# Kernel optimization log

Hardware: AMD Instinct MI355X
Metric: run time of the kernel (lower is better)

Reference implementation:

```python
import jax, jax.numpy as jnp
import numpy as np

N = 30000        # nodes
E = 600000       # edges
R = 32           # relations
NB = 30          # num_bases
D = 128          # entity_dim == hidden_dim == output_dim
H = 8            # heads, head dim C = D // H = 16
NUM_ENT = 100000
NGRAPH = 16      # graphs in batch
L = 2            # num_rgcn_layers == num_transformer_layers
EPS = 1e-5


def _ln(x, g, b):
    mu = x.mean(-1, keepdims=True)
    var = ((x - mu) ** 2).mean(-1, keepdims=True)
    return (x - mu) * jax.lax.rsqrt(var + EPS) * g + b


def setup_inputs() -> dict:
    key = jax.random.key(0)
    ks = iter(jax.random.split(key, 48))

    def nrm(shape, s=0.05):
        return jax.random.normal(next(ks), shape, jnp.float32) * s

    inp = {}
    inp["node_ids"] = jax.random.randint(next(ks), (N,), 0, NUM_ENT)
    inp["edge_index"] = jax.random.randint(next(ks), (2, E), 0, N)
    inp["edge_type"] = jax.random.randint(next(ks), (E,), 0, R)
    inp["batch"] = jnp.sort(jax.random.randint(next(ks), (N,), 0, NGRAPH))
    inp["entity_emb"] = nrm((NUM_ENT, D)).at[0].set(0.0)  # padding_idx=0
    inp["rel_emb"] = nrm((R, D)).at[0].set(0.0)           # padding_idx=0
    inp["rgcn_comp"] = nrm((L, R, NB))
    inp["rgcn_bases"] = nrm((L, NB, D, D))
    inp["rgcn_root"] = nrm((L, D, D))
    inp["rgcn_bias"] = jnp.zeros((L, D), jnp.float32)
    inp["rgcn_ln_g"] = jnp.ones((L, D), jnp.float32)
    inp["rgcn_ln_b"] = jnp.zeros((L, D), jnp.float32)
    inp["tr_wq"] = nrm((L, D, D)); inp["tr_bq"] = jnp.zeros((L, D), jnp.float32)
    inp["tr_wk"] = nrm((L, D, D)); inp["tr_bk"] = jnp.zeros((L, D), jnp.float32)
    inp["tr_wv"] = nrm((L, D, D)); inp["tr_bv"] = jnp.zeros((L, D), jnp.float32)
    inp["tr_we"] = nrm((L, D, D))                          # lin_edge (bias=False in PyG)
    inp["tr_wskip"] = nrm((L, D, D)); inp["tr_bskip"] = jnp.zeros((L, D), jnp.float32)
    inp["tr_ln_g"] = jnp.ones((L, D), jnp.float32)
    inp["tr_ln_b"] = jnp.zeros((L, D), jnp.float32)
    return inp


def reference(node_ids, edge_index, edge_type, batch, entity_emb, rel_emb,
              rgcn_comp, rgcn_bases, rgcn_root, rgcn_bias, rgcn_ln_g, rgcn_ln_b,
              tr_wq, tr_bq, tr_wk, tr_bk, tr_wv, tr_bv, tr_we, tr_wskip, tr_bskip,
              tr_ln_g, tr_ln_b):
    src, tgt = edge_index[0], edge_index[1]
    C = D // H
    x = entity_emb[node_ids]            # [N, D]
    edge_attr = rel_emb[edge_type]      # [E, D]

    # ---- RGCN layers: basis decomposition, mean aggregation per (target, relation) ----
    seg = tgt * R + edge_type
    cnt = jax.ops.segment_sum(jnp.ones((E,), jnp.float32), seg, num_segments=N * R)
    inv = jnp.where(cnt > 0, 1.0 / jnp.maximum(cnt, 1.0), 0.0)   # [N*R]
    for l in range(L):
        agg = jax.ops.segment_sum(x[src], seg, num_segments=N * R)   # [N*R, D]
        agg = (agg * inv[:, None]).reshape(N, R, D)
        w = jnp.einsum('rb,bio->rio', rgcn_comp[l], rgcn_bases[l])   # [R, D, D]
        x = jnp.einsum('nri,rio->no', agg, w) + x @ rgcn_root[l] + rgcn_bias[l]
        x = jax.nn.relu(_ln(x, rgcn_ln_g[l], rgcn_ln_b[l]))          # dropout = identity (eval)

    # ---- TransformerConv layers: edge-conditioned multi-head attention ----
    for l in range(L):
        q = (x @ tr_wq[l] + tr_bq[l]).reshape(N, H, C)
        k = (x @ tr_wk[l] + tr_bk[l]).reshape(N, H, C)
        v = (x @ tr_wv[l] + tr_bv[l]).reshape(N, H, C)
        e = (edge_attr @ tr_we[l]).reshape(E, H, C)
        kj = k[src] + e                                              # [E, H, C]
        vj = v[src] + e
        alpha = jnp.einsum('ehc,ehc->eh', q[tgt], kj) / np.float32(np.sqrt(C))
        m = jax.ops.segment_max(alpha, tgt, num_segments=N)          # [N, H]
        a = jnp.exp(alpha - m[tgt])
        denom = jax.ops.segment_sum(a, tgt, num_segments=N)
        a = a / jnp.maximum(denom[tgt], 1e-16)                       # softmax per target node
        out = jax.ops.segment_sum((vj * a[:, :, None]).reshape(E, D), tgt, num_segments=N)
        out = out + x @ tr_wskip[l] + tr_bskip[l]                    # root/skip connection
        out = jax.nn.relu(_ln(out, tr_ln_g[l], tr_ln_b[l]))          # dropout = identity (eval)
        x = x + out                                                  # dims match -> residual

    cnt_g = jax.ops.segment_sum(jnp.ones((N,), jnp.float32), batch, num_segments=NGRAPH)
    graph_emb = jax.ops.segment_sum(x, batch, num_segments=NGRAPH) / jnp.maximum(cnt_g, 1.0)[:, None]
    return x, graph_emb
```

## Files before the change

### kernel.cpp

```cpp
#include <hip/hip_runtime.h>

#define NN 30000
#define NE 600000
#define RR 32
#define NBASE 30
#define NG 16

typedef long long i64;
typedef unsigned short ushort;
typedef short bf16x8 __attribute__((ext_vector_type(8)));
typedef float f32x4 __attribute__((ext_vector_type(4)));

__device__ __forceinline__ ushort f2bf(float f){
  unsigned u = __float_as_uint(f);
  u += 0x7fffu + ((u >> 16) & 1u);
  return (ushort)(u >> 16);
}
__device__ __forceinline__ float bf2f(ushort u){
  return __uint_as_float(((unsigned)u) << 16);
}
__device__ __forceinline__ unsigned pk2(float a, float b){
  return (unsigned)f2bf(a) | ((unsigned)f2bf(b) << 16);
}

__global__ void k_gather(const float* __restrict__ emb, const int* __restrict__ ids,
                         float* __restrict__ x, ushort* __restrict__ xb){
  int t = blockIdx.x*256 + threadIdx.x;
  if (t >= NN*32) return;
  int n = t >> 5, c = t & 31;
  float4 v = ((const float4*)emb)[(i64)ids[n]*32 + c];
  ((float4*)x)[(i64)n*32 + c] = v;
  *(uint2*)&xb[(i64)n*128 + c*4] = make_uint2(pk2(v.x, v.y), pk2(v.z, v.w));
}

__global__ void k_cnt(const int* __restrict__ tgt, const int* __restrict__ ety,
                      float* __restrict__ cnt){
  int e = blockIdx.x*256 + threadIdx.x;
  if (e >= NE) return;
  atomicAdd(&cnt[(i64)tgt[e]*RR + ety[e]], 1.0f);
}

__global__ void k_hist_blk(const int* __restrict__ ety, int* __restrict__ hist){
  __shared__ int lh[RR];
  if (threadIdx.x < RR) lh[threadIdx.x] = 0;
  __syncthreads();
  int e0 = blockIdx.x*2048 + threadIdx.x;
  #pragma unroll
  for (int i = 0; i < 8; i++){
    int e = e0 + i*256;
    if (e < NE) atomicAdd(&lh[ety[e]], 1);
  }
  __syncthreads();
  if (threadIdx.x < RR){
    int v = lh[threadIdx.x];
    if (v) atomicAdd(&hist[threadIdx.x], v);
  }
}

__global__ void k_scan(const int* __restrict__ hist, int* __restrict__ base,
                       int* __restrict__ cursor, int* __restrict__ pb,
                       int* __restrict__ pb64){
  if (threadIdx.x != 0 || blockIdx.x != 0) return;
  int s = 0, p = 0, p64 = 0;
  for (int r = 0; r < RR; r++){
    base[r] = s; cursor[r] = s; pb[r] = p; pb64[r] = p64;
    s += hist[r]; p += (hist[r] + 127) >> 7; p64 += (hist[r] + 63) >> 6;
  }
  base[RR] = s; pb[RR] = p; pb64[RR] = p64;
}

__global__ __launch_bounds__(256) void k_scatter_blk(const int* __restrict__ ety,
    int* __restrict__ cursor, int* __restrict__ eord){
  __shared__ int lh[RR];
  __shared__ int lb[RR];
  if (threadIdx.x < RR) lh[threadIdx.x] = 0;
  __syncthreads();
  int e0 = blockIdx.x*2048 + threadIdx.x;
  #pragma unroll
  for (int i = 0; i < 8; i++){
    int e = e0 + i*256;
    if (e < NE) atomicAdd(&lh[ety[e]], 1);
  }
  __syncthreads();
  if (threadIdx.x < RR){
    int c = lh[threadIdx.x];
    lb[threadIdx.x] = c ? atomicAdd(&cursor[threadIdx.x], c) : 0;
  }
  __syncthreads();
  if (threadIdx.x < RR) lh[threadIdx.x] = 0;
  __syncthreads();
  #pragma unroll
  for (int i = 0; i < 8; i++){
    int e = e0 + i*256;
    if (e < NE){
      int r = ety[e];
      int loc = atomicAdd(&lh[r], 1);
      eord[lb[r] + loc] = e;
    }
  }
}

__global__ void k_hist2(const int* __restrict__ etgt, int* __restrict__ hist2){
  int e = blockIdx.x*256 + threadIdx.x;
  if (e >= NE) return;
  atomicAdd(&hist2[etgt[e]], 1);
}

__global__ __launch_bounds__(1024) void k_scan2(const int* __restrict__ hist2,
    int* __restrict__ rowptr, int* __restrict__ cursor2){
  __shared__ int s[1024];
  int t = threadIdx.x;
  int base = t*30;
  int loc[30];
  int sum = 0;
  #pragma unroll
  for (int i = 0; i < 30; i++){
    int v = (base+i < NN) ? hist2[base+i] : 0;
    loc[i] = sum; sum += v;
  }
  s[t] = sum; __syncthreads();
  for (int off = 1; off < 1024; off <<= 1){
    int v = (t >= off) ? s[t-off] : 0;
    __syncthreads();
    s[t] += v;
    __syncthreads();
  }
  int excl = (t > 0) ? s[t-1] : 0;
  #pragma unroll
  for (int i = 0; i < 30; i++){
    int idx = base + i;
    if (idx <= NN){
      rowptr[idx] = excl + loc[i];
      if (idx < NN) cursor2[idx] = excl + loc[i];
    }
  }
}

__global__ void k_scatter2(const int* __restrict__ etgt, const int* __restrict__ esrc,
                           const int* __restrict__ ety, int* __restrict__ cursor2,
                           int2* __restrict__ se2, int* __restrict__ pos2){
  int e = blockIdx.x*256 + threadIdx.x;
  if (e >= NE) return;
  int q = atomicAdd(&cursor2[etgt[e]], 1);
  se2[q] = make_int2(esrc[e], ety[e]);
  pos2[e] = q;
  if (e == 0){
    se2[NE]     = make_int2(0, 0);
    se2[NE + 1] = make_int2(0, 0);
  }
}

__global__ void k_prep(const int* __restrict__ eord, const int* __restrict__ esrc,
                       const int* __restrict__ etgt, const int* __restrict__ ety,
                       const int* __restrict__ pos2, const float* __restrict__ cnt,
                       int* __restrict__ sg_src, int* __restrict__ sg_p2,
                       float* __restrict__ sg_inv){
  int s = blockIdx.x*256 + threadIdx.x;
  if (s >= NE) return;
  int eid = eord[s];
  sg_src[s] = esrc[eid];
  sg_p2[s]  = pos2[eid];
  sg_inv[s] = 1.0f / cnt[(i64)etgt[eid]*RR + ety[eid]];
}

__global__ void k_basis(const float* __restrict__ comp, const float* __restrict__ bases,
                        float* __restrict__ wT, ushort* __restrict__ wTb){
  int t = blockIdx.x*256 + threadIdx.x;
  int r = t >> 14, rem = t & 16383, c = rem >> 7, kk = rem & 127;
  float acc = 0.f;
  for (int b = 0; b < NBASE; b++)
    acc += comp[r*NBASE + b] * bases[(i64)b*16384 + kk*128 + c];
  wT[t] = acc;
  wTb[t] = f2bf(acc);
}

__global__ void k_tw(const float* __restrict__ root, const float* __restrict__ wq,
                     const float* __restrict__ wk, const float* __restrict__ wv,
                     const float* __restrict__ wsk, ushort* __restrict__ out){
  int z = blockIdx.y;
  const float* srcs[5] = {root, wq, wk, wv, wsk};
  const float* S = srcs[z >> 1] + (i64)(z & 1)*16384;
  int idx = blockIdx.x*256 + threadIdx.x;
  int c = idx >> 7, kk = idx & 127;
  out[(i64)z*16384 + idx] = f2bf(S[kk*128 + c]);
}


__global__ __launch_bounds__(256, 4) void k_mm_mfma(const ushort* __restrict__ xb,
    const ushort* __restrict__ wTb, const float* __restrict__ bias,
    float* __restrict__ Y, int nrows){
  __shared__ ushort Xs[16384];
  int t = threadIdx.x;
  int row0 = blockIdx.x * 128;
  for (int i = t; i < 2048; i += 256){
    int row = i >> 4, c = i & 15;
    int gr = min(row0 + row, nrows - 1);
    *(uint4*)((char*)Xs + row*256 + ((c*16) ^ ((row&7)<<4))) =
        *(const uint4*)((const char*)(xb + (i64)gr*128) + c*16);
  }
  __syncthreads();
  int w = t >> 6, l = t & 63;
  int wm = w >> 1, wn = w & 1;
  int lrow = l & 15, lg = l >> 4;
  int swz = (lrow & 7) << 4;
  const char* pX = (const char*)Xs + (wm*64 + lrow)*256;
  const char* pW = (const char*)wTb + (wn*64 + lrow)*256 + 16*lg;
  f32x4 acc[4][4] = {};
  #pragma unroll
  for (int ks = 0; ks < 4; ks++){
    int kb = (16*lg + 64*ks) ^ swz;
    bf16x8 a[4], bx[4];
    #pragma unroll
    for (int ns = 0; ns < 4; ns++) a[ns]  = *(const bf16x8*)(pW + ns*4096 + 64*ks);
    #pragma unroll
    for (int ms = 0; ms < 4; ms++) bx[ms] = *(const bf16x8*)(pX + ms*4096 + kb);
    #pragma unroll
    for (int ms = 0; ms < 4; ms++)
      #pragma unroll
      for (int ns = 0; ns < 4; ns++)
        acc[ms][ns] = __builtin_amdgcn_mfma_f32_16x16x32_bf16(a[ns], bx[ms], acc[ms][ns], 0, 0, 0);
  }
  #pragma unroll
  for (int ms = 0; ms < 4; ms++){
    int m = row0 + wm*64 + ms*16 + lrow;
    if (m >= nrows) continue;
    #pragma unroll
    for (int ns = 0; ns < 4; ns++){
      int n0 = wn*64 + ns*16 + 4*lg;
      float4 bv = *(const float4*)&bias[n0];
      f32x4 v = acc[ms][ns];
      *(float4*)&Y[(i64)m*128 + n0] =
          make_float4(v[0]+bv.x, v[1]+bv.y, v[2]+bv.z, v[3]+bv.w);
    }
  }
}

__global__ __launch_bounds__(256, 4) void k_mm4(const ushort* __restrict__ xb,
    const ushort* __restrict__ wTb, int layer,
    const float* __restrict__ biq, const float* __restrict__ bik,
    const float* __restrict__ biv, const float* __restrict__ bisk,
    ushort* __restrict__ qo, ushort* __restrict__ ko, ushort* __restrict__ vo,
    float* __restrict__ z, int nrows){
  __shared__ ushort Xs[16384];
  int t = threadIdx.x;
  int row0 = blockIdx.x * 128;
  for (int i = t; i < 2048; i += 256){
    int row = i >> 4, c = i & 15;
    int gr = min(row0 + row, nrows - 1);
    *(uint4*)((char*)Xs + row*256 + ((c*16) ^ ((row&7)<<4))) =
        *(const uint4*)((const char*)(xb + (i64)gr*128) + c*16);
  }
  __syncthreads();
  int w = t >> 6, l = t & 63;
  int wm = w >> 1, wn = w & 1;
  int lrow = l & 15, lg = l >> 4;
  int swz = (lrow & 7) << 4;
  const char* pX = (const char*)Xs + (wm*64 + lrow)*256;
  const float* biases[4] = {biq, bik, biv, bisk};
  ushort* outs[3] = {qo, ko, vo};
  #pragma unroll 1
  for (int arr = 0; arr < 4; arr++){
    const char* pW = (const char*)(wTb + (i64)(2 + 2*arr + layer)*16384)
                     + (wn*64 + lrow)*256 + 16*lg;
    f32x4 acc[4][4] = {};
    #pragma unroll
    for (int ks = 0; ks < 4; ks++){
      int kb = (16*lg + 64*ks) ^ swz;
      bf16x8 a[4], bx[4];
      #pragma unroll
      for (int ns = 0; ns < 4; ns++) a[ns]  = *(const bf16x8*)(pW + ns*4096 + 64*ks);
      #pragma unroll
      for (int ms = 0; ms < 4; ms++) bx[ms] = *(const bf16x8*)(pX + ms*4096 + kb);
      #pragma unroll
      for (int ms = 0; ms < 4; ms++)
        #pragma unroll
        for (int ns = 0; ns < 4; ns++)
          acc[ms][ns] = __builtin_amdgcn_mfma_f32_16x16x32_bf16(a[ns], bx[ms], acc[ms][ns], 0, 0, 0);
    }
    const float* bias = biases[arr];
    #pragma unroll
    for (int ms = 0; ms < 4; ms++){
      int m = row0 + wm*64 + ms*16 + lrow;
      if (m >= nrows) continue;
      #pragma unroll
      for (int ns = 0; ns < 4; ns++){
        int n0 = wn*64 + ns*16 + 4*lg;
        float4 bv = *(const float4*)&bias[n0];
        f32x4 v = acc[ms][ns];
        if (arr < 3){
          *(uint2*)&outs[arr][(i64)m*128 + n0] =
              make_uint2(pk2(v[0]+bv.x, v[1]+bv.y), pk2(v[2]+bv.z, v[3]+bv.w));
        } else {
          *(float4*)&z[(i64)m*128 + n0] =
              make_float4(v[0]+bv.x, v[1]+bv.y, v[2]+bv.z, v[3]+bv.w);
        }
      }
    }
  }
}

__global__ __launch_bounds__(256, 4) void k_edge_mfma(
    const int* __restrict__ sg_src, const int* __restrict__ sg_p2,
    const float* __restrict__ sg_inv, const int* __restrict__ hist,
    const int* __restrict__ base, const int* __restrict__ pb,
    const ushort* __restrict__ xb, const ushort* __restrict__ wb,
    ushort* __restrict__ y){
  __shared__ ushort Xs[16384];
  __shared__ int s_src[128];
  __shared__ int s_p2[128];
  __shared__ float s_inv[128];
  int b = blockIdx.x;
  int r = -1;
  #pragma unroll 1
  for (int i = 0; i < RR; i++){
    if (b >= pb[i] && b < pb[i+1]) { r = i; break; }
  }
  if (r < 0) return;
  int chunk = b - pb[r];
  int rowbase = base[r] + chunk*128;
  int nvalid = min(128, hist[r] - chunk*128);
  int t = threadIdx.x;
  if (t < 128){
    bool valid = t < nvalid;
    int slot = rowbase + (valid ? t : 0);
    s_src[t] = sg_src[slot];
    s_p2[t]  = valid ? sg_p2[slot] : NE;
    s_inv[t] = valid ? sg_inv[slot] : 0.0f;
  }
  __syncthreads();
  for (int i = t; i < 2048; i += 256){
    int row = i >> 4, c = i & 15;
    *(uint4*)((char*)Xs + row*256 + ((c*16) ^ ((row&7)<<4))) =
        *(const uint4*)((const char*)(xb + (i64)s_src[row]*128) + c*16);
  }
  __syncthreads();
  int w = t >> 6, l = t & 63;
  int wm = w >> 1, wn = w & 1;
  int lrow = l & 15, lg = l >> 4;
  int swz = (lrow & 7) << 4;
  const char* pX = (const char*)Xs + (wm*64 + lrow)*256;
  const char* pW = (const char*)(wb + (i64)r*16384) + (wn*64 + lrow)*256 + 16*lg;
  f32x4 acc[4][4] = {};
  #pragma unroll
  for (int ks = 0; ks < 4; ks++){
    int kb = (16*lg + 64*ks) ^ swz;
    bf16x8 a[4], bx[4];
    #pragma unroll
    for (int ns = 0; ns < 4; ns++) a[ns]  = *(const bf16x8*)(pW + ns*4096 + 64*ks);
    #pragma unroll
    for (int ms = 0; ms < 4; ms++) bx[ms] = *(const bf16x8*)(pX + ms*4096 + kb);
    #pragma unroll
    for (int ms = 0; ms < 4; ms++)
      #pragma unroll
      for (int ns = 0; ns < 4; ns++)
        acc[ms][ns] = __builtin_amdgcn_mfma_f32_16x16x32_bf16(a[ns], bx[ms], acc[ms][ns], 0, 0, 0);
  }
  __syncthreads();
  #pragma unroll
  for (int ms = 0; ms < 4; ms++){
    int m = wm*64 + ms*16 + lrow;
    float sc = s_inv[m];
    int msk = (m & 7) << 4;
    #pragma unroll
    for (int ns = 0; ns < 4; ns++){
      int n0 = wn*64 + ns*16 + 4*lg;
      f32x4 v = acc[ms][ns];
      *(uint2*)((char*)Xs + m*256 + ((n0*2) ^ msk)) =
          make_uint2(pk2(v[0]*sc, v[1]*sc), pk2(v[2]*sc, v[3]*sc));
    }
  }
  __syncthreads();
  for (int i = t; i < 2048; i += 256){
    int row = i >> 4, c = i & 15;
    uint4 v = *(const uint4*)((const char*)Xs + row*256 + ((c*16) ^ ((row&7)<<4)));
    *(uint4*)&y[(i64)s_p2[row]*128 + c*8] = v;
  }
}

__global__ __launch_bounds__(256) void k_edge_atomic(const int* __restrict__ esrc,
    const int* __restrict__ etgt, const int* __restrict__ eord,
    const int* __restrict__ hist, const int* __restrict__ base,
    const int* __restrict__ pb, const float* __restrict__ cnt,
    const float* __restrict__ x, const float* __restrict__ wT,
    float* __restrict__ z){
  __shared__ float Xs[64][132];
  __shared__ int s_src[64];
  __shared__ int s_tgt[64];
  __shared__ float s_inv[64];
  int b = blockIdx.x;
  int r = -1;
  #pragma unroll 1
  for (int i = 0; i < RR; i++){
    if (b >= pb[i] && b < pb[i+1]) { r = i; break; }
  }
  if (r < 0) return;
  int chunk = b - pb[r];
  int rowbase = base[r] + chunk*64;
  int cnt_r = hist[r];
  if (threadIdx.x < 64){
    int i = threadIdx.x;
    bool valid = (chunk*64 + i) < cnt_r;
    int eid = valid ? eord[rowbase + i] : 0;
    int sv = valid ? esrc[eid] : 0;
    int tv = valid ? etgt[eid] : 0;
    s_src[i] = sv; s_tgt[i] = tv;
    s_inv[i] = valid ? (1.0f / cnt[(i64)tv*RR + r]) : 0.0f;
  }
  __syncthreads();
  for (int idx = threadIdx.x; idx < 64*32; idx += 256){
    int rr = idx >> 5, c4 = idx & 31;
    *(float4*)&Xs[rr][c4*4] = ((const float4*)x)[(i64)s_src[rr]*32 + c4];
  }
  __syncthreads();
  const float* W = wT + (i64)r*16384;
  int m = threadIdx.x & 15, cg = threadIdx.x >> 4;
  float acc[4][8] = {};
  #pragma unroll 2
  for (int k4 = 0; k4 < 128; k4 += 4){
    float4 xv[4], wv[8];
    #pragma unroll
    for (int i = 0; i < 4; i++) xv[i] = *(float4*)&Xs[m + 16*i][k4];
    #pragma unroll
    for (int j = 0; j < 8; j++) wv[j] = *(const float4*)&W[(i64)(cg + 16*j)*128 + k4];
    #pragma unroll
    for (int i = 0; i < 4; i++)
      #pragma unroll
      for (int j = 0; j < 8; j++)
        acc[i][j] += xv[i].x*wv[j].x + xv[i].y*wv[j].y + xv[i].z*wv[j].z + xv[i].w*wv[j].w;
  }
  #pragma unroll
  for (int i = 0; i < 4; i++){
    int rr = m + 16*i;
    float sc = s_inv[rr];
    i64 o = (i64)s_tgt[rr]*128;
    #pragma unroll
    for (int j = 0; j < 8; j++)
      atomicAdd(&z[o + cg + 16*j], acc[i][j]*sc);
  }
}

__global__ void k_seg(const int* __restrict__ rowptr, const ushort* __restrict__ y,
                      const float* __restrict__ z, const float* __restrict__ g,
                      const float* __restrict__ b, float* __restrict__ x,
                      ushort* __restrict__ xb){
  int t = (blockIdx.x*256 + threadIdx.x) >> 6;
  int l = threadIdx.x & 63;
  if (t >= NN) return;
  int q0 = rowptr[t], q1 = rowptr[t+1];
  float ax = 0.f, ay = 0.f;
  for (int q = q0; q < q1; q++){
    ushort2 u = *(const ushort2*)&y[(i64)q*128 + 2*l];
    ax += bf2f(u.x); ay += bf2f(u.y);
  }
  float2 zv = *(const float2*)&z[(i64)t*128 + 2*l];
  float tx = ax + zv.x, ty = ay + zv.y;
  float s = tx + ty;
  #pragma unroll
  for (int o = 1; o < 64; o <<= 1) s += __shfl_xor(s, o);
  float mu = s * 0.0078125f;
  float dx = tx - mu, dy = ty - mu;
  float s2 = dx*dx + dy*dy;
  #pragma unroll
  for (int o = 1; o < 64; o <<= 1) s2 += __shfl_xor(s2, o);
  float rs = rsqrtf(s2 * 0.0078125f + 1e-5f);
  float2 gg = *(const float2*)&g[2*l];
  float2 bb = *(const float2*)&b[2*l];
  float o0 = fmaxf(dx*rs*gg.x + bb.x, 0.f);
  float o1 = fmaxf(dy*rs*gg.y + bb.y, 0.f);
  *(float2*)&x[(i64)t*128 + 2*l] = make_float2(o0, o1);
  *(unsigned*)&xb[(i64)t*128 + 2*l] = pk2(o0, o1);
}

__global__ void k_lnrelu(const float* __restrict__ z, const float* __restrict__ g,
                         const float* __restrict__ b, float* __restrict__ xo,
                         ushort* __restrict__ xb){
  int w = (blockIdx.x*256 + threadIdx.x) >> 6;
  int l = threadIdx.x & 63;
  if (w >= NN) return;
  float2 v = *(const float2*)&z[(i64)w*128 + 2*l];
  float s = v.x + v.y;
  #pragma unroll
  for (int o = 1; o < 64; o <<= 1) s += __shfl_xor(s, o);
  float mu = s * 0.0078125f;
  float dx = v.x - mu, dy = v.y - mu;
  float s2 = dx*dx + dy*dy;
  #pragma unroll
  for (int o = 1; o < 64; o <<= 1) s2 += __shfl_xor(s2, o);
  float rs = rsqrtf(s2 * 0.0078125f + 1e-5f);
  float2 gg = *(const float2*)&g[2*l];
  float2 bb = *(const float2*)&b[2*l];
  float o0 = fmaxf(dx*rs*gg.x + bb.x, 0.f);
  float o1 = fmaxf(dy*rs*gg.y + bb.y, 0.f);
  *(float2*)&xo[(i64)w*128 + 2*l] = make_float2(o0, o1);
  *(unsigned*)&xb[(i64)w*128 + 2*l] = pk2(o0, o1);
}

__global__ void k_ew(const float* __restrict__ rel, const float* __restrict__ we,
                     float* __restrict__ ew){
  int t = blockIdx.x*256 + threadIdx.x;
  int r = t >> 7, c = t & 127;
  float acc = 0.f;
  for (int k = 0; k < 128; k++) acc += rel[r*128 + k] * we[k*128 + c];
  ew[t] = acc;
}

__global__ __launch_bounds__(256) void k_attn(const int2* __restrict__ se2,
    const int* __restrict__ rowptr,
    const ushort* __restrict__ qbb, const ushort* __restrict__ kbb,
    const ushort* __restrict__ vbb, const float* __restrict__ ew,
    const float* __restrict__ sk, const float* __restrict__ g,
    const float* __restrict__ b, float* __restrict__ x, ushort* __restrict__ xb){
  __shared__ float sew[RR*128];
  __shared__ float part[4][3][64];
  for (int i = threadIdx.x; i < RR*32; i += 256)
    ((float4*)sew)[i] = ((const float4*)ew)[i];
  __syncthreads();
  int wid = threadIdx.x >> 6;
  int half = wid & 1;
  int t = blockIdx.x*2 + (wid >> 1);
  int l = threadIdx.x & 63;
  int q0 = rowptr[t], q1 = rowptr[t+1];
  unsigned qu = *(const unsigned*)&qbb[(i64)t*128 + 2*l];
  float qx = bf2f((ushort)qu) * 0.25f, qy = bf2f((ushort)(qu >> 16)) * 0.25f;
  float den = 0.f, ox = 0.f, oy = 0.f;
  int qs = q0 + half;
  if (qs < q1){
    int2 sr = se2[qs];
    unsigned ku = *(const unsigned*)&kbb[(i64)sr.x*128 + 2*l];
    unsigned vu = *(const unsigned*)&vbb[(i64)sr.x*128 + 2*l];
    int r = sr.y;
    for (int q = qs; q < q1; q += 2){
      int2 srn = se2[q + 2];
      unsigned kun = *(const unsigned*)&kbb[(i64)srn.x*128 + 2*l];
      unsigned vun = *(const unsigned*)&vbb[(i64)srn.x*128 + 2*l];
      float2 ev = *(const float2*)&sew[r*128 + 2*l];
      float kx = bf2f((ushort)ku) + ev.x, ky = bf2f((ushort)(ku >> 16)) + ev.y;
      float p = qx*kx + qy*ky;
      p += __shfl_xor(p, 1); p += __shfl_xor(p, 2); p += __shfl_xor(p, 4);
      float wgt = __expf(p);
      den += wgt;
      ox += wgt*(bf2f((ushort)vu) + ev.x);
      oy += wgt*(bf2f((ushort)(vu >> 16)) + ev.y);
      ku = kun; vu = vun; r = srn.y;
    }
  }
  part[wid][0][l] = ox; part[wid][1][l] = oy; part[wid][2][l] = den;
  __syncthreads();
  if (half) return;
  ox  += part[wid^1][0][l];
  oy  += part[wid^1][1][l];
  den += part[wid^1][2][l];
  float dn = fmaxf(den, 1e-16f);
  float2 zv = *(const float2*)&sk[(i64)t*128 + 2*l];
  float tx = ox/dn + zv.x, ty = oy/dn + zv.y;
  float s = tx + ty;
  #pragma unroll
  for (int o = 1; o < 64; o <<= 1) s += __shfl_xor(s, o);
  float mu = s * 0.0078125f;
  float dx = tx - mu, dy = ty - mu;
  float s2 = dx*dx + dy*dy;
  #pragma unroll
  for (int o = 1; o < 64; o <<= 1) s2 += __shfl_xor(s2, o);
  float rs = rsqrtf(s2 * 0.0078125f + 1e-5f);
  float2 gg = *(const float2*)&g[2*l];
  float2 bb = *(const float2*)&b[2*l];
  float o0 = fmaxf(dx*rs*gg.x + bb.x, 0.f);
  float o1 = fmaxf(dy*rs*gg.y + bb.y, 0.f);
  float2 xv = *(const float2*)&x[(i64)t*128 + 2*l];
  float nx = xv.x + o0, ny = xv.y + o1;
  *(float2*)&x[(i64)t*128 + 2*l] = make_float2(nx, ny);
  *(unsigned*)&xb[(i64)t*128 + 2*l] = pk2(nx, ny);
}

__global__ void k_copy(const float* __restrict__ x, float* __restrict__ out){
  int t = blockIdx.x*256 + threadIdx.x;
  if (t >= NN*32) return;
  ((float4*)out)[t] = ((const float4*)x)[t];
}

__global__ void k_cntg(const int* __restrict__ batch, float* __restrict__ cntg){
  __shared__ int lh[NG];
  if (threadIdx.x < NG) lh[threadIdx.x] = 0;
  __syncthreads();
  int n = blockIdx.x*256 + threadIdx.x;
  if (n < NN) atomicAdd(&lh[batch[n]], 1);
  __syncthreads();
  if (threadIdx.x < NG){
    int v = lh[threadIdx.x];
    if (v) atomicAdd(&cntg[threadIdx.x], (float)v);
  }
}

__global__ void k_pool(const float* __restrict__ x, const int* __restrict__ batch,
                       float* __restrict__ gsum){
  __shared__ float acc[NG*128];
  for (int i = threadIdx.x; i < NG*128; i += 256) acc[i] = 0.f;
  __syncthreads();
  int per = (NN + gridDim.x - 1) / gridDim.x;
  int n0 = blockIdx.x*per, n1 = min(n0 + per, NN);
  int sub = threadIdx.x >> 5, c4 = threadIdx.x & 31;
  for (int n = n0 + sub; n < n1; n += 8){
    int g = batch[n];
    float4 xv = ((const float4*)x)[(i64)n*32 + c4];
    atomicAdd(&acc[g*128 + c4*4 + 0], xv.x);
    atomicAdd(&acc[g*128 + c4*4 + 1], xv.y);
    atomicAdd(&acc[g*128 + c4*4 + 2], xv.z);
    atomicAdd(&acc[g*128 + c4*4 + 3], xv.w);
  }
  __syncthreads();
  for (int i = threadIdx.x; i < NG*128; i += 256) atomicAdd(&gsum[i], acc[i]);
}

__global__ void k_poolfin(const float* __restrict__ gsum, const float* __restrict__ cntg,
                          float* __restrict__ gout){
  int t = blockIdx.x*256 + threadIdx.x;
  int g = t >> 7;
  gout[t] = gsum[t] / fmaxf(cntg[g], 1.0f);
}

extern "C" void kernel_launch(void* const* d_in, const int* in_sizes, int n_in,
                              void* d_out, int out_size, void* d_ws, size_t ws_size,
                              hipStream_t stream) {
  const int*   node_ids = (const int*)d_in[0];
  const int*   eidx  = (const int*)d_in[1];
  const int*   esrc  = eidx;
  const int*   etgt  = eidx + NE;
  const int*   ety   = (const int*)d_in[2];
  const int*   batch = (const int*)d_in[3];
  const float* ent   = (const float*)d_in[4];
  const float* rel   = (const float*)d_in[5];
  const float* comp  = (const float*)d_in[6];
  const float* bases = (const float*)d_in[7];
  const float* root  = (const float*)d_in[8];
  const float* rbias = (const float*)d_in[9];
  const float* rlng  = (const float*)d_in[10];
  const float* rlnb  = (const float*)d_in[11];
  const float* wq    = (const float*)d_in[12];
  const float* bq    = (const float*)d_in[13];
  const float* wk    = (const float*)d_in[14];
  const float* bk    = (const float*)d_in[15];
  const float* wv    = (const float*)d_in[16];
  const float* bv    = (const float*)d_in[17];
  const float* we    = (const float*)d_in[18];
  const float* wsk   = (const float*)d_in[19];
  const float* bsk   = (const float*)d_in[20];
  const float* tlng  = (const float*)d_in[21];
  const float* tlnb  = (const float*)d_in[22];
  float* out = (float*)d_out;

  char* wp = (char*)d_ws;
  auto alloc = [&](size_t bytes)->void*{
    void* p = (void*)wp;
    wp += (bytes + 255) & ~(size_t)255;
    return p;
  };
  float*    x     = (float*)alloc((size_t)NN*128*4);
  ushort*   xb    = (ushort*)alloc((size_t)NN*128*2);
  float*    z     = (float*)alloc((size_t)NN*128*4);
  ushort*   qbb   = (ushort*)alloc((size_t)NN*128*2);
  ushort*   kbb   = (ushort*)alloc((size_t)NN*128*2);
  ushort*   vbb   = (ushort*)alloc((size_t)NN*128*2);
  float*    cnt   = (float*)alloc((size_t)NN*RR*4);
  float*    wbT   = (float*)alloc((size_t)RR*16384*4);
  ushort*   wbTb  = (ushort*)alloc((size_t)RR*16384*2);
  ushort*   wTb   = (ushort*)alloc((size_t)10*16384*2);
  float*    ew    = (float*)alloc((size_t)RR*128*4);
  int*      eord  = (int*)alloc((size_t)NE*4);
  int*      pos2  = (int*)alloc((size_t)NE*4);
  int2*     se2   = (int2*)alloc((size_t)(NE + 2)*8);
  int*      sg_src= (int*)alloc((size_t)NE*4);
  int*      sg_p2 = (int*)alloc((size_t)NE*4);
  float*    sg_inv= (float*)alloc((size_t)NE*4);
  int*      hist  = (int*)alloc(RR*4);
  int*      base  = (int*)alloc((RR+1)*4);
  int*      cursor= (int*)alloc(RR*4);
  int*      pb    = (int*)alloc((RR+1)*4);
  int*      pb64  = (int*)alloc((RR+1)*4);
  int*      hist2 = (int*)alloc((size_t)NN*4);
  int*      rowptr= (int*)alloc((size_t)(NN+1)*4);
  int*      cursor2=(int*)alloc((size_t)NN*4);
  float*    cntg  = (float*)alloc(NG*4);
  float*    gsum  = (float*)alloc((size_t)NG*128*4);
  size_t ybytes = (size_t)(NE + 8)*128*2;
  ushort*   y     = (ushort*)alloc(ybytes);
  bool fast = ((char*)y + ybytes) <= ((char*)d_ws + ws_size);

  dim3 B(256);

  hipMemsetAsync(cnt, 0, (size_t)NN*RR*4, stream);
  hipMemsetAsync(hist, 0, RR*4, stream);
  hipMemsetAsync(hist2, 0, (size_t)NN*4, stream);

  k_gather<<<3750, B, 0, stream>>>(ent, node_ids, x, xb);
  k_cnt<<<2344, B, 0, stream>>>(etgt, ety, cnt);
  k_hist_blk<<<294, B, 0, stream>>>(ety, hist);
  k_scan<<<1, 1, 0, stream>>>(hist, base, cursor, pb, pb64);
  k_scatter_blk<<<294, B, 0, stream>>>(ety, cursor, eord);
  k_hist2<<<2344, B, 0, stream>>>(etgt, hist2);
  k_scan2<<<1, 1024, 0, stream>>>(hist2, rowptr, cursor2);
  k_scatter2<<<2344, B, 0, stream>>>(etgt, esrc, ety, cursor2, se2, pos2);
  k_prep<<<2344, B, 0, stream>>>(eord, esrc, etgt, ety, pos2, cnt, sg_src, sg_p2, sg_inv);
  k_tw<<<dim3(64,10), B, 0, stream>>>(root, wq, wk, wv, wsk, wTb);

  for (int l = 0; l < 2; l++){
    k_basis<<<2048, B, 0, stream>>>(comp + l*RR*NBASE, bases + (i64)l*NBASE*16384, wbT, wbTb);
    k_mm_mfma<<<235, B, 0, stream>>>(xb, wTb + (i64)(0 + l)*16384, rbias + l*128, z, NN);
    if (fast){
      k_edge_mfma<<<4720, B, 0, stream>>>(sg_src, sg_p2, sg_inv, hist, base, pb, xb, wbTb, y);
      k_seg<<<7500, B, 0, stream>>>(rowptr, y, z, rlng + l*128, rlnb + l*128, x, xb);
    } else {
      k_edge_atomic<<<9407, B, 0, stream>>>(esrc, etgt, eord, hist, base, pb64, cnt, x, wbT, z);
      k_lnrelu<<<7500, B, 0, stream>>>(z, rlng + l*128, rlnb + l*128, x, xb);
    }
  }

  for (int l = 0; l < 2; l++){
    k_ew<<<16, B, 0, stream>>>(rel, we + (i64)l*16384, ew);
    k_mm4<<<235, B, 0, stream>>>(xb, wTb, l, bq + l*128, bk + l*128, bv + l*128,
                                 bsk + l*128, qbb, kbb, vbb, z, NN);
    k_attn<<<15000, B, 0, stream>>>(se2, rowptr, qbb, kbb, vbb, ew, z,
                                    tlng + l*128, tlnb + l*128, x, xb);
  }

  k_copy<<<3750, B, 0, stream>>>(x, out);
  hipMemsetAsync(gsum, 0, (size_t)NG*128*4, stream);
  hipMemsetAsync(cntg, 0, NG*4, stream);
  k_cntg<<<118, B, 0, stream>>>(batch, cntg);
  k_pool<<<120, B, 0, stream>>>(x, batch, gsum);
  k_poolfin<<<8, B, 0, stream>>>(gsum, cntg, out + (i64)NN*128);
}
```

Baseline: 899.1 us.

## Fuse preprocessing kernels, deepen attention prefetch, write final layer to output

Merges the count, relation histogram and target histogram kernels into one pass, folds the small relation scan into the node scan, and folds the sorted-edge gather into the relation scatter kernel, cutting several launches and extra passes over the edge arrays. The attention kernel now prefetches four edges ahead instead of one to hide gather latency, with the padding of se2 grown to match. The last attention layer writes straight to the output buffer, which removes the final copy kernel. The deeper prefetch raises register use in the attention kernel.

After: 865.5 us. 3.7% less time.

```diff
diff --git a/kernel.cpp b/kernel.cpp
--- a/kernel.cpp
+++ b/kernel.cpp
@@ -33,14 +33,9 @@
   *(uint2*)&xb[(i64)n*128 + c*4] = make_uint2(pk2(v.x, v.y), pk2(v.z, v.w));
 }
 
-__global__ void k_cnt(const int* __restrict__ tgt, const int* __restrict__ ety,
-                      float* __restrict__ cnt){
-  int e = blockIdx.x*256 + threadIdx.x;
-  if (e >= NE) return;
-  atomicAdd(&cnt[(i64)tgt[e]*RR + ety[e]], 1.0f);
-}
-
-__global__ void k_hist_blk(const int* __restrict__ ety, int* __restrict__ hist){
+__global__ __launch_bounds__(256) void k_stats(const int* __restrict__ etgt,
+    const int* __restrict__ ety, float* __restrict__ cnt,
+    int* __restrict__ hist, int* __restrict__ hist2){
   __shared__ int lh[RR];
   if (threadIdx.x < RR) lh[threadIdx.x] = 0;
   __syncthreads();
@@ -48,7 +43,12 @@
   #pragma unroll
   for (int i = 0; i < 8; i++){
     int e = e0 + i*256;
-    if (e < NE) atomicAdd(&lh[ety[e]], 1);
+    if (e < NE){
+      int tgt = etgt[e], r = ety[e];
+      atomicAdd(&lh[r], 1);
+      atomicAdd(&hist2[tgt], 1);
+      atomicAdd(&cnt[(i64)tgt*RR + r], 1.0f);
+    }
   }
   __syncthreads();
   if (threadIdx.x < RR){
@@ -57,65 +57,26 @@
   }
 }
 
-__global__ void k_scan(const int* __restrict__ hist, int* __restrict__ base,
-                       int* __restrict__ cursor, int* __restrict__ pb,
-                       int* __restrict__ pb64){
-  if (threadIdx.x != 0 || blockIdx.x != 0) return;
-  int s = 0, p = 0, p64 = 0;
-  for (int r = 0; r < RR; r++){
-    base[r] = s; cursor[r] = s; pb[r] = p; pb64[r] = p64;
-    s += hist[r]; p += (hist[r] + 127) >> 7; p64 += (hist[r] + 63) >> 6;
-  }
-  base[RR] = s; pb[RR] = p; pb64[RR] = p64;
-}
-
-__global__ __launch_bounds__(256) void k_scatter_blk(const int* __restrict__ ety,
-    int* __restrict__ cursor, int* __restrict__ eord){
-  __shared__ int lh[RR];
-  __shared__ int lb[RR];
-  if (threadIdx.x < RR) lh[threadIdx.x] = 0;
-  __syncthreads();
-  int e0 = blockIdx.x*2048 + threadIdx.x;
-  #pragma unroll
-  for (int i = 0; i < 8; i++){
-    int e = e0 + i*256;
-    if (e < NE) atomicAdd(&lh[ety[e]], 1);
-  }
-  __syncthreads();
-  if (threadIdx.x < RR){
-    int c = lh[threadIdx.x];
-    lb[threadIdx.x] = c ? atomicAdd(&cursor[threadIdx.x], c) : 0;
-  }
-  __syncthreads();
-  if (threadIdx.x < RR) lh[threadIdx.x] = 0;
-  __syncthreads();
-  #pragma unroll
-  for (int i = 0; i < 8; i++){
-    int e = e0 + i*256;
-    if (e < NE){
-      int r = ety[e];
-      int loc = atomicAdd(&lh[r], 1);
-      eord[lb[r] + loc] = e;
-    }
-  }
-}
-
-__global__ void k_hist2(const int* __restrict__ etgt, int* __restrict__ hist2){
-  int e = blockIdx.x*256 + threadIdx.x;
-  if (e >= NE) return;
-  atomicAdd(&hist2[etgt[e]], 1);
-}
-
 __global__ __launch_bounds__(1024) void k_scan2(const int* __restrict__ hist2,
-    int* __restrict__ rowptr, int* __restrict__ cursor2){
+    int* __restrict__ rowptr, int* __restrict__ cursor2,
+    const int* __restrict__ hist, int* __restrict__ base,
+    int* __restrict__ cursor, int* __restrict__ pb, int* __restrict__ pb64){
+  int t = threadIdx.x;
+  if (t == 0){
+    int s = 0, p = 0, p64 = 0;
+    for (int r = 0; r < RR; r++){
+      base[r] = s; cursor[r] = s; pb[r] = p; pb64[r] = p64;
+      s += hist[r]; p += (hist[r] + 127) >> 7; p64 += (hist[r] + 63) >> 6;
+    }
+    base[RR] = s; pb[RR] = p; pb64[RR] = p64;
+  }
   __shared__ int s[1024];
-  int t = threadIdx.x;
-  int base = t*30;
+  int bse = t*30;
   int loc[30];
   int sum = 0;
   #pragma unroll
   for (int i = 0; i < 30; i++){
-    int v = (base+i < NN) ? hist2[base+i] : 0;
+    int v = (bse+i < NN) ? hist2[bse+i] : 0;
     loc[i] = sum; sum += v;
   }
   s[t] = sum; __syncthreads();
@@ -128,7 +89,7 @@
   int excl = (t > 0) ? s[t-1] : 0;
   #pragma unroll
   for (int i = 0; i < 30; i++){
-    int idx = base + i;
+    int idx = bse + i;
     if (idx <= NN){
       rowptr[idx] = excl + loc[i];
       if (idx < NN) cursor2[idx] = excl + loc[i];
@@ -144,23 +105,45 @@
   int q = atomicAdd(&cursor2[etgt[e]], 1);
   se2[q] = make_int2(esrc[e], ety[e]);
   pos2[e] = q;
-  if (e == 0){
-    se2[NE]     = make_int2(0, 0);
-    se2[NE + 1] = make_int2(0, 0);
-  }
-}
-
-__global__ void k_prep(const int* __restrict__ eord, const int* __restrict__ esrc,
-                       const int* __restrict__ etgt, const int* __restrict__ ety,
-                       const int* __restrict__ pos2, const float* __restrict__ cnt,
-                       int* __restrict__ sg_src, int* __restrict__ sg_p2,
-                       float* __restrict__ sg_inv){
-  int s = blockIdx.x*256 + threadIdx.x;
-  if (s >= NE) return;
-  int eid = eord[s];
-  sg_src[s] = esrc[eid];
-  sg_p2[s]  = pos2[eid];
-  sg_inv[s] = 1.0f / cnt[(i64)etgt[eid]*RR + ety[eid]];
+  if (e < 8) se2[NE + e] = make_int2(0, 0);
+}
+
+__global__ __launch_bounds__(256) void k_scatter_blk(const int* __restrict__ ety,
+    const int* __restrict__ esrc, const int* __restrict__ etgt,
+    const int* __restrict__ pos2, const float* __restrict__ cnt,
+    int* __restrict__ cursor, int* __restrict__ eord,
+    int* __restrict__ sg_src, int* __restrict__ sg_p2, float* __restrict__ sg_inv){
+  __shared__ int lh[RR];
+  __shared__ int lb[RR];
+  if (threadIdx.x < RR) lh[threadIdx.x] = 0;
+  __syncthreads();
+  int e0 = blockIdx.x*2048 + threadIdx.x;
+  #pragma unroll
+  for (int i = 0; i < 8; i++){
+    int e = e0 + i*256;
+    if (e < NE) atomicAdd(&lh[ety[e]], 1);
+  }
+  __syncthreads();
+  if (threadIdx.x < RR){
+    int c = lh[threadIdx.x];
+    lb[threadIdx.x] = c ? atomicAdd(&cursor[threadIdx.x], c) : 0;
+  }
+  __syncthreads();
+  if (threadIdx.x < RR) lh[threadIdx.x] = 0;
+  __syncthreads();
+  #pragma unroll
+  for (int i = 0; i < 8; i++){
+    int e = e0 + i*256;
+    if (e < NE){
+      int r = ety[e];
+      int loc = atomicAdd(&lh[r], 1);
+      int slot = lb[r] + loc;
+      eord[slot]   = e;
+      sg_src[slot] = esrc[e];
+      sg_p2[slot]  = pos2[e];
+      sg_inv[slot] = 1.0f / cnt[(i64)etgt[e]*RR + r];
+    }
+  }
 }
 
 __global__ void k_basis(const float* __restrict__ comp, const float* __restrict__ bases,
@@ -509,7 +492,8 @@
     const ushort* __restrict__ qbb, const ushort* __restrict__ kbb,
     const ushort* __restrict__ vbb, const float* __restrict__ ew,
     const float* __restrict__ sk, const float* __restrict__ g,
-    const float* __restrict__ b, float* __restrict__ x, ushort* __restrict__ xb){
+    const float* __restrict__ b, const float* __restrict__ xin,
+    float* __restrict__ xout, ushort* __restrict__ xb){
   __shared__ float sew[RR*128];
   __shared__ float part[4][3][64];
   for (int i = threadIdx.x; i < RR*32; i += 256)
@@ -525,23 +509,30 @@
   float den = 0.f, ox = 0.f, oy = 0.f;
   int qs = q0 + half;
   if (qs < q1){
-    int2 sr = se2[qs];
-    unsigned ku = *(const unsigned*)&kbb[(i64)sr.x*128 + 2*l];
-    unsigned vu = *(const unsigned*)&vbb[(i64)sr.x*128 + 2*l];
-    int r = sr.y;
+    int2 s0 = se2[qs], s1 = se2[qs+2], s2 = se2[qs+4], s3 = se2[qs+6];
+    unsigned ku0 = *(const unsigned*)&kbb[(i64)s0.x*128 + 2*l];
+    unsigned vu0 = *(const unsigned*)&vbb[(i64)s0.x*128 + 2*l];
+    unsigned ku1 = *(const unsigned*)&kbb[(i64)s1.x*128 + 2*l];
+    unsigned vu1 = *(const unsigned*)&vbb[(i64)s1.x*128 + 2*l];
+    unsigned ku2 = *(const unsigned*)&kbb[(i64)s2.x*128 + 2*l];
+    unsigned vu2 = *(const unsigned*)&vbb[(i64)s2.x*128 + 2*l];
+    unsigned ku3 = *(const unsigned*)&kbb[(i64)s3.x*128 + 2*l];
+    unsigned vu3 = *(const unsigned*)&vbb[(i64)s3.x*128 + 2*l];
     for (int q = qs; q < q1; q += 2){
-      int2 srn = se2[q + 2];
-      unsigned kun = *(const unsigned*)&kbb[(i64)srn.x*128 + 2*l];
-      unsigned vun = *(const unsigned*)&vbb[(i64)srn.x*128 + 2*l];
-      float2 ev = *(const float2*)&sew[r*128 + 2*l];
-      float kx = bf2f((ushort)ku) + ev.x, ky = bf2f((ushort)(ku >> 16)) + ev.y;
+      int2 s4 = se2[q + 8];
+      unsigned ku4 = *(const unsigned*)&kbb[(i64)s4.x*128 + 2*l];
+      unsigned vu4 = *(const unsigned*)&vbb[(i64)s4.x*128 + 2*l];
+      float2 ev = *(const float2*)&sew[s0.y*128 + 2*l];
+      float kx = bf2f((ushort)ku0) + ev.x, ky = bf2f((ushort)(ku0 >> 16)) + ev.y;
       float p = qx*kx + qy*ky;
       p += __shfl_xor(p, 1); p += __shfl_xor(p, 2); p += __shfl_xor(p, 4);
       float wgt = __expf(p);
       den += wgt;
-      ox += wgt*(bf2f((ushort)vu) + ev.x);
-      oy += wgt*(bf2f((ushort)(vu >> 16)) + ev.y);
-      ku = kun; vu = vun; r = srn.y;
+      ox += wgt*(bf2f((ushort)vu0) + ev.x);
+      oy += wgt*(bf2f((ushort)(vu0 >> 16)) + ev.y);
+      s0 = s1; s1 = s2; s2 = s3; s3 = s4;
+      ku0 = ku1; ku1 = ku2; ku2 = ku3; ku3 = ku4;
+      vu0 = vu1; vu1 = vu2; vu2 = vu3; vu3 = vu4;
     }
   }
   part[wid][0][l] = ox; part[wid][1][l] = oy; part[wid][2][l] = den;
@@ -566,16 +557,10 @@
   float2 bb = *(const float2*)&b[2*l];
   float o0 = fmaxf(dx*rs*gg.x + bb.x, 0.f);
   float o1 = fmaxf(dy*rs*gg.y + bb.y, 0.f);
-  float2 xv = *(const float2*)&x[(i64)t*128 + 2*l];
+  float2 xv = *(const float2*)&xin[(i64)t*128 + 2*l];
   float nx = xv.x + o0, ny = xv.y + o1;
-  *(float2*)&x[(i64)t*128 + 2*l] = make_float2(nx, ny);
+  *(float2*)&xout[(i64)t*128 + 2*l] = make_float2(nx, ny);
   *(unsigned*)&xb[(i64)t*128 + 2*l] = pk2(nx, ny);
-}
-
-__global__ void k_copy(const float* __restrict__ x, float* __restrict__ out){
-  int t = blockIdx.x*256 + threadIdx.x;
-  if (t >= NN*32) return;
-  ((float4*)out)[t] = ((const float4*)x)[t];
 }
 
 __global__ void k_cntg(const int* __restrict__ batch, float* __restrict__ cntg){
@@ -667,7 +652,7 @@
   float*    ew    = (float*)alloc((size_t)RR*128*4);
   int*      eord  = (int*)alloc((size_t)NE*4);
   int*      pos2  = (int*)alloc((size_t)NE*4);
-  int2*     se2   = (int2*)alloc((size_t)(NE + 2)*8);
+  int2*     se2   = (int2*)alloc((size_t)(NE + 8)*8);
   int*      sg_src= (int*)alloc((size_t)NE*4);
   int*      sg_p2 = (int*)alloc((size_t)NE*4);
   float*    sg_inv= (float*)alloc((size_t)NE*4);
@@ -692,14 +677,11 @@
   hipMemsetAsync(hist2, 0, (size_t)NN*4, stream);
 
   k_gather<<<3750, B, 0, stream>>>(ent, node_ids, x, xb);
-  k_cnt<<<2344, B, 0, stream>>>(etgt, ety, cnt);
-  k_hist_blk<<<294, B, 0, stream>>>(ety, hist);
-  k_scan<<<1, 1, 0, stream>>>(hist, base, cursor, pb, pb64);
-  k_scatter_blk<<<294, B, 0, stream>>>(ety, cursor, eord);
-  k_hist2<<<2344, B, 0, stream>>>(etgt, hist2);
-  k_scan2<<<1, 1024, 0, stream>>>(hist2, rowptr, cursor2);
+  k_stats<<<294, B, 0, stream>>>(etgt, ety, cnt, hist, hist2);
+  k_scan2<<<1, 1024, 0, stream>>>(hist2, rowptr, cursor2, hist, base, cursor, pb, pb64);
   k_scatter2<<<2344, B, 0, stream>>>(etgt, esrc, ety, cursor2, se2, pos2);
-  k_prep<<<2344, B, 0, stream>>>(eord, esrc, etgt, ety, pos2, cnt, sg_src, sg_p2, sg_inv);
+  k_scatter_blk<<<294, B, 0, stream>>>(ety, esrc, etgt, pos2, cnt, cursor, eord,
+                                       sg_src, sg_p2, sg_inv);
   k_tw<<<dim3(64,10), B, 0, stream>>>(root, wq, wk, wv, wsk, wTb);
 
   for (int l = 0; l < 2; l++){
@@ -719,13 +701,13 @@
     k_mm4<<<235, B, 0, stream>>>(xb, wTb, l, bq + l*128, bk + l*128, bv + l*128,
                                  bsk + l*128, qbb, kbb, vbb, z, NN);
     k_attn<<<15000, B, 0, stream>>>(se2, rowptr, qbb, kbb, vbb, ew, z,
-                                    tlng + l*128, tlnb + l*128, x, xb);
-  }
-
-  k_copy<<<3750, B, 0, stream>>>(x, out);
+                                    tlng + l*128, tlnb + l*128, x,
+                                    (l == 1) ? out : x, xb);
+  }
+
   hipMemsetAsync(gsum, 0, (size_t)NG*128*4, stream);
   hipMemsetAsync(cntg, 0, NG*4, stream);
   k_cntg<<<118, B, 0, stream>>>(batch, cntg);
-  k_pool<<<120, B, 0, stream>>>(x, batch, gsum);
+  k_pool<<<120, B, 0, stream>>>(out, batch, gsum);
   k_poolfin<<<8, B, 0, stream>>>(gsum, cntg, out + (i64)NN*128);
 }
```
